# Optimization experiments

Hardware: AMD Instinct MI355X
Metric: run time of the kernel (lower is better)

Reference implementation:

```python
import jax, jax.numpy as jnp
import numpy as np

N_HEAD = 16
T_THRESHOLD = 0.001


def setup_inputs() -> dict:
    key = jax.random.key(0)
    k_x, k_wa, k_ba, k_wp, k_bp = jax.random.split(key, 5)
    B, P, L, R = 8, 1024, 4, 256
    C = L * R  # n_embd = 1024
    s = 1.0 / np.sqrt(C)
    return {
        "x": jax.random.normal(k_x, (B, P, L, R), dtype=jnp.float32),
        "w_attn": jax.random.normal(k_wa, (C, 3 * C), dtype=jnp.float32) * s,
        "b_attn": jax.random.normal(k_ba, (3 * C,), dtype=jnp.float32) * 0.01,
        "w_proj": jax.random.normal(k_wp, (C, C), dtype=jnp.float32) * s,
        "b_proj": jax.random.normal(k_bp, (C,), dtype=jnp.float32) * 0.01,
    }


def reference(x, w_attn, b_attn, w_proj, b_proj):
    B, P, L, R = x.shape
    C = L * R
    H = N_HEAD
    hd = C // H
    xf = x.reshape(B, P, C)                      # (B, T, C)
    qkv = xf @ w_attn + b_attn                   # (B, T, 3C)
    q, k, v = jnp.split(qkv, 3, axis=-1)
    # (B, H, T, hd)
    q = q.reshape(B, P, H, hd).transpose(0, 2, 1, 3)
    k = k.reshape(B, P, H, hd).transpose(0, 2, 1, 3)
    v = v.reshape(B, P, H, hd).transpose(0, 2, 1, 3)
    att = jnp.einsum("bhqd,bhkd->bhqk", q, k) * (1.0 / np.sqrt(hd))
    att = jax.nn.softmax(att, axis=-1)
    att = jax.nn.relu(att - T_THRESHOLD)         # post-softmax thresholding
    y = jnp.einsum("bhqk,bhkd->bhqd", att, v)    # (B, H, T, hd)
    y = y.transpose(0, 2, 1, 3).reshape(B, P, C)
    y = y @ w_proj + b_proj
    return y.reshape(B, P, L, R)
```

## Files before the change

### kernel.cpp

```cpp
#include <hip/hip_runtime.h>


typedef _Float16 half8 __attribute__((ext_vector_type(8)));
typedef _Float16 half4_t __attribute__((ext_vector_type(4)));
typedef float floatx4 __attribute__((ext_vector_type(4)));

__device__ __forceinline__ void gl2lds16(const void* gsrc, void* lds) {
    __builtin_amdgcn_global_load_lds(
        (const __attribute__((address_space(1))) unsigned int*)gsrc,
        (__attribute__((address_space(3))) unsigned int*)lds,
        16, 0, 0);
}

__global__ __launch_bounds__(256) void conv_x(const float4* __restrict__ in,
                                              _Float16* __restrict__ out, int n4) {
    int idx = blockIdx.x * blockDim.x + threadIdx.x;
    int stride = gridDim.x * blockDim.x;
    for (int i = idx; i < n4; i += stride) {
        float4 v = in[i];
        half4_t h = { (_Float16)v.x, (_Float16)v.y, (_Float16)v.z, (_Float16)v.w };
        *(half4_t*)(out + (size_t)i * 4) = h;
    }
}

__global__ __launch_bounds__(256) void tconv(const float* __restrict__ in,
                                             _Float16* __restrict__ out, int R, int C) {
    __shared__ _Float16 t[64 * 65];
    int bx = blockIdx.x, by = blockIdx.y;
#pragma unroll
    for (int it = 0; it < 16; ++it) {
        int idx = it * 256 + threadIdx.x;
        int r = idx >> 6, c = idx & 63;
        t[c * 65 + r] = (_Float16)in[(size_t)(by * 64 + r) * C + bx * 64 + c];
    }
    __syncthreads();
#pragma unroll
    for (int it = 0; it < 16; ++it) {
        int idx = it * 256 + threadIdx.x;
        int rn = idx >> 6, ck = idx & 63;
        out[(size_t)(bx * 64 + rn) * R + by * 64 + ck] = t[rn * 65 + ck];
    }
}


#define GBAR __builtin_amdgcn_s_barrier()
#define WLGKM do { asm volatile("s_waitcnt lgkmcnt(0)" ::: "memory"); } while (0)
#define WVM2  do { asm volatile("s_waitcnt vmcnt(2)"   ::: "memory"); } while (0)
#define WVM0  do { asm volatile("s_waitcnt vmcnt(0)"   ::: "memory"); } while (0)

#define LDA(buf, rg)                                                                          \
    do {                                                                                      \
        _Pragma("unroll") for (int i = 0; i < 2; ++i) {                                       \
            int r_ = wm * 64 + ((rg) * 2 + i) * 16 + l15;                                     \
            _Pragma("unroll") for (int kk = 0; kk < 2; ++kk)                                  \
                a[i][kk] = *(const half8*)(sA + (buf) * 32768 + r_ * 128 +                    \
                                           ((((kk << 2) + quad) ^ (r_ & 7)) << 4));           \
        }                                                                                     \
    } while (0)

#define LDB(buf, cg, bb)                                                                      \
    do {                                                                                      \
        _Pragma("unroll") for (int j = 0; j < 2; ++j) {                                       \
            int r_ = wn * 64 + ((cg) * 2 + j) * 16 + l15;                                     \
            _Pragma("unroll") for (int kk = 0; kk < 2; ++kk)                                  \
                bb[j][kk] = *(const half8*)(sB + (buf) * 16384 + r_ * 128 +                   \
                                            ((((kk << 2) + quad) ^ (r_ & 7)) << 4));          \
        }                                                                                     \
    } while (0)

#define MMA(rg, cg, bb)                                                                       \
    do {                                                                                      \
        __builtin_amdgcn_s_setprio(1);                                                        \
        _Pragma("unroll") for (int kk = 0; kk < 2; ++kk)                                      \
            _Pragma("unroll") for (int i = 0; i < 2; ++i)                                     \
                _Pragma("unroll") for (int j = 0; j < 2; ++j)                                  \
                    acc[(rg) * 2 + i][(cg) * 2 + j] = __builtin_amdgcn_mfma_f32_16x16x32_f16( \
                        a[i][kk], bb[j][kk], acc[(rg) * 2 + i][(cg) * 2 + j], 0, 0, 0);       \
        __builtin_amdgcn_s_setprio(0);                                                        \
    } while (0)

template <bool SPLIT3>
__global__ __launch_bounds__(512, 2) void gemm8p(const _Float16* __restrict__ A,
                                                 const _Float16* __restrict__ BT,
                                                 const float* __restrict__ bias,
                                                 void* __restrict__ o0, void* __restrict__ o1,
                                                 void* __restrict__ o2, int N) {
    __shared__ __attribute__((aligned(16))) char lds[98304];
    char* sA = lds;
    char* sB = lds + 65536;
    int tid = threadIdx.x;
    int W = tid >> 6, lane = tid & 63, quad = lane >> 4, l15 = lane & 15;
    int wm = W >> 1, wn = W & 1;
    int m0 = blockIdx.y * 256, n0 = blockIdx.x * 128;

    auto stA = [&](int buf, int half, int k0) {
#pragma unroll
        for (int rnd = 0; rnd < 2; ++rnd) {
            int c = rnd * 512 + tid;
            int row = c >> 3;
            int q = (c & 7) ^ (row & 7);
            const _Float16* src = A + (size_t)(m0 + half * 128 + row) * 1024 + k0 + q * 8;
            int off = __builtin_amdgcn_readfirstlane(buf * 32768 + half * 16384 +
                                                     rnd * 8192 + (W << 10));
            gl2lds16(src, sA + off);
        }
    };
    auto stB = [&](int buf, int half, int k0) {
        int row = tid >> 3;
        int q = (tid & 7) ^ (row & 7);
        const _Float16* src = BT + (size_t)(n0 + half * 64 + row) * 1024 + k0 + q * 8;
        int off = __builtin_amdgcn_readfirstlane(buf * 16384 + half * 8192 + (W << 10));
        gl2lds16(src, sB + off);
    };

    half8 a[2][2], b0[2][2], b1[2][2];
    floatx4 acc[4][4] = {};

    stA(0, 0, 0); stA(0, 1, 0);
    stB(0, 0, 0); stB(0, 1, 0);
    stB(1, 0, 64); stB(1, 1, 64);
    WVM2;
    GBAR;

#pragma unroll 1
    for (int t = 0; t < 16; t += 2) {
        int k1 = (t + 1) << 6;
        int k2 = ((t + 2) & 15) << 6;
        int k3 = ((t + 3) & 15) << 6;
        LDA(0, 0); LDB(0, 0, b0); stA(1, 0, k1);
        GBAR; WLGKM; MMA(0, 0, b0); GBAR;
        LDB(0, 1, b1); stA(1, 1, k1);
        GBAR; WLGKM; MMA(0, 1, b1); GBAR;
        LDA(0, 1); stB(0, 0, k2);
        GBAR; WLGKM; MMA(1, 1, b1); GBAR;
        stB(0, 1, k2); WVM2;
        GBAR; WLGKM; MMA(1, 0, b0); GBAR;
        LDA(1, 0); LDB(1, 0, b0); stA(0, 0, k2);
        GBAR; WLGKM; MMA(0, 0, b0); GBAR;
        LDB(1, 1, b1); stA(0, 1, k2);
        GBAR; WLGKM; MMA(0, 1, b1); GBAR;
        LDA(1, 1); stB(1, 0, k3);
        GBAR; WLGKM; MMA(1, 1, b1); GBAR;
        stB(1, 1, k3); WVM2;
        GBAR; WLGKM; MMA(1, 0, b0); GBAR;
    }

    if constexpr (!SPLIT3) {
#pragma unroll
        for (int cf = 0; cf < 4; ++cf) {
            int gn = n0 + wn * 64 + cf * 16 + l15;
            float bv = bias[gn];
#pragma unroll
            for (int rf = 0; rf < 4; ++rf) {
                int gmBase = m0 + wm * 64 + rf * 16 + quad * 4;
#pragma unroll
                for (int r = 0; r < 4; ++r)
                    ((float*)o0)[(size_t)(gmBase + r) * N + gn] = acc[rf][cf][r] + bv;
            }
        }
    } else {
        WVM0;
        GBAR;
        int sec = n0 >> 10;
        int nb = n0 & 1023;
        int b = m0 >> 10;
        int tb = m0 & 1023;
        _Float16* qno = (_Float16*)o0;
        _Float16* kPo = (_Float16*)o1;
        _Float16* vPo = (_Float16*)o2;
        if (sec == 2) {
#pragma unroll
            for (int cf = 0; cf < 4; ++cf) {
                int n = wn * 64 + cf * 16 + l15;
                float bv = bias[n0 + n];
#pragma unroll
                for (int rf = 0; rf < 4; ++rf) {
                    int m = wm * 64 + rf * 16 + quad * 4;
                    half4_t h4;
#pragma unroll
                    for (int r = 0; r < 4; ++r) h4[r] = (_Float16)(acc[rf][cf][r] + bv);
                    *(half4_t*)(lds + n * 528 + ((m >> 3) << 4) + (m & 7) * 2) = h4;
                }
            }
            __syncthreads();
            int l15v = tid & 15;
            int moct = W * 4 + ((tid >> 4) & 3);
            int t = tb + moct * 8;
            int kbv = (t >> 5) & 31, quad_v = (t >> 3) & 3;
#pragma unroll
            for (int i = 0; i < 8; ++i) {
                int hh = i >> 2, cf = i & 3;
                int n = hh * 64 + cf * 16 + l15v;
                half8 v = *(const half8*)(lds + n * 528 + (moct << 4));
                int gcol = nb + n;
                int h = gcol >> 6, d = gcol & 63;
                size_t chunk = (size_t)((b * 16 + h) * 32 + kbv) * 256 +
                               (d >> 4) * 64 + quad_v * 16 + (d & 15);
                *(half8*)(vPo + chunk * 8) = v;
            }
        } else {
#pragma unroll
            for (int cf = 0; cf < 4; ++cf) {
                int n = wn * 64 + cf * 16 + l15;
                float bv = bias[n0 + n];
                int nbyte = ((n >> 3) << 4) + (n & 7) * 2;
#pragma unroll
                for (int rf = 0; rf < 4; ++rf) {
                    int m = wm * 64 + rf * 16 + quad * 4;
#pragma unroll
                    for (int r = 0; r < 4; ++r)
                        *(_Float16*)(lds + (m + r) * 272 + nbyte) =
                            (_Float16)(acc[rf][cf][r] + bv);
                }
            }
            __syncthreads();
            if (sec == 0) {
                int noct = tid & 15;
#pragma unroll
                for (int i = 0; i < 8; ++i) {
                    int m = i * 32 + (tid >> 4);
                    half8 v = *(const half8*)(lds + m * 272 + (noct << 4));
                    *(half8*)(qno + (size_t)(b * 1024 + tb + m) * 1024 + nb + noct * 8) = v;
                }
            } else {
                int l15k = tid & 15, noct = (tid >> 4) & 15;
#pragma unroll
                for (int i = 0; i < 8; ++i) {
                    int mb = i * 2 + (tid >> 8);
                    int m = mb * 16 + l15k;
                    half8 v = *(const half8*)(lds + m * 272 + (noct << 4));
                    int gcol = nb + noct * 8;
                    int h = gcol >> 6, d0 = gcol & 63;
                    int t = tb + m;
                    size_t chunk = (size_t)((b * 16 + h) * 64 + (t >> 4)) * 128 +
                                   (d0 >> 5) * 64 + ((d0 >> 3) & 3) * 16 + l15k;
                    *(half8*)(kPo + chunk * 8) = v;
                }
            }
        }
    }
}

__device__ __forceinline__ int esw(int row, int colByte) {
    return row * 2048 + (colByte ^ ((row & 7) << 4));
}

__global__ __launch_bounds__(512, 4) void attn(const _Float16* __restrict__ qn,
                                               const _Float16* __restrict__ kP,
                                               const _Float16* __restrict__ vP,
                                               _Float16* __restrict__ y) {
    __shared__ __attribute__((aligned(16))) _Float16 E[32 * 1024];
    __shared__ float lsum[8][32];
    char* Eb = (char*)E;
    int tid = threadIdx.x;
    int W = tid >> 6, lane = tid & 63, quad = lane >> 4, l15 = lane & 15;
    int flat = blockIdx.y * 32 + blockIdx.x;
    int swz = (flat & 7) * 512 + (flat >> 3);
    int qt = swz & 31, bh = swz >> 5;
    int b = bh >> 4, h = bh & 15;
    int q0 = qt * 32;

    half8 bq[2][2];
#pragma unroll
    for (int nf = 0; nf < 2; ++nf)
#pragma unroll
        for (int ks = 0; ks < 2; ++ks)
            bq[nf][ks] = *(const half8*)(qn + (size_t)(b * 1024 + q0 + nf * 16 + l15) * 1024 +
                                         h * 64 + ks * 32 + quad * 8);

    float lpart[2] = {0.f, 0.f};
#pragma unroll 4
    for (int mt = 0; mt < 8; ++mt) {
        int kb = W * 8 + mt;
        const _Float16* kp = kP + ((size_t)(bh * 64 + kb) * 128 + lane) * 8;
        half8 ak0 = *(const half8*)(kp);
        half8 ak1 = *(const half8*)(kp + 512);
#pragma unroll
        for (int nf = 0; nf < 2; ++nf) {
            floatx4 s = {};
            s = __builtin_amdgcn_mfma_f32_16x16x32_f16(ak0, bq[nf][0], s, 0, 0, 0);
            s = __builtin_amdgcn_mfma_f32_16x16x32_f16(ak1, bq[nf][1], s, 0, 0, 0);
            half4_t h4;
#pragma unroll
            for (int r = 0; r < 4; ++r) {
                float e = __expf(fminf(s[r] * 0.125f, 10.0f));
                lpart[nf] += e;
                h4[r] = (_Float16)e;
            }
            int q = nf * 16 + l15;
            int kbyte = (W * 128 + mt * 16 + quad * 4) * 2;
            *(half4_t*)(Eb + q * 2048 + (kbyte ^ ((q & 7) << 4))) = h4;
        }
    }
#pragma unroll
    for (int nf = 0; nf < 2; ++nf) {
        lpart[nf] += __shfl_xor(lpart[nf], 16);
        lpart[nf] += __shfl_xor(lpart[nf], 32);
    }
    if (lane < 16) {
        lsum[W][l15] = lpart[0];
        lsum[W][16 + l15] = lpart[1];
    }
    __syncthreads();

    half8 inv8[2], t8, z8;
#pragma unroll
    for (int j = 0; j < 8; ++j) { t8[j] = (_Float16)(-0.001f); z8[j] = (_Float16)0.f; }
#pragma unroll
    for (int rf = 0; rf < 2; ++rf) {
        float l = 0.f;
#pragma unroll
        for (int w = 0; w < 8; ++w) l += lsum[w][rf * 16 + l15];
        _Float16 invh = (_Float16)(1.0f / l);
#pragma unroll
        for (int j = 0; j < 8; ++j) inv8[rf][j] = invh;
    }

    floatx4 acc[2][4] = {};
#pragma unroll
    for (int kt = 0; kt < 4; ++kt) {
        int kk = W * 128 + kt * 32;
        half8 ap[2];
#pragma unroll
        for (int rf = 0; rf < 2; ++rf) {
            ap[rf] = *(const half8*)(Eb + esw(rf * 16 + l15, (kk + quad * 8) * 2));
            ap[rf] = ap[rf] * inv8[rf] + t8;
            ap[rf] = __builtin_elementwise_max(ap[rf], z8);
        }
        const _Float16* vbase = vP + ((size_t)(bh * 32 + (W * 4 + kt)) * 256 + lane) * 8;
        half8 bv[4];
#pragma unroll
        for (int cf = 0; cf < 4; ++cf)
            bv[cf] = *(const half8*)(vbase + cf * 512);
#pragma unroll
        for (int rf = 0; rf < 2; ++rf)
#pragma unroll
            for (int cf = 0; cf < 4; ++cf)
                acc[rf][cf] = __builtin_amdgcn_mfma_f32_16x16x32_f16(ap[rf], bv[cf], acc[rf][cf], 0, 0, 0);
    }
    __syncthreads();

    float* red = (float*)E;
#pragma unroll
    for (int rf = 0; rf < 2; ++rf)
#pragma unroll
        for (int cf = 0; cf < 4; ++cf)
#pragma unroll
            for (int r = 0; r < 4; ++r)
                red[W * 2048 + (rf * 16 + quad * 4 + r) * 64 + cf * 16 + l15] = acc[rf][cf][r];
    __syncthreads();
    {
        int e4 = tid * 4;
        int r = e4 >> 6, c = e4 & 63;
        floatx4 s = {};
#pragma unroll
        for (int w = 0; w < 8; ++w) s += *(const floatx4*)(red + w * 2048 + e4);
        half4_t hv = { (_Float16)s[0], (_Float16)s[1], (_Float16)s[2], (_Float16)s[3] };
        *(half4_t*)(y + (size_t)(b * 1024 + q0 + r) * 1024 + h * 64 + c) = hv;
    }
}

extern "C" void kernel_launch(void* const* d_in, const int* in_sizes, int n_in,
                              void* d_out, int out_size, void* d_ws, size_t ws_size,
                              hipStream_t stream) {
    const float* x  = (const float*)d_in[0];
    const float* wa = (const float*)d_in[1];
    const float* ba = (const float*)d_in[2];
    const float* wp = (const float*)d_in[3];
    const float* bp = (const float*)d_in[4];
    float* out = (float*)d_out;

    char* ws = (char*)d_ws;
    _Float16* y   = (_Float16*)(ws);
    _Float16* qn  = (_Float16*)(ws + 16777216);
    _Float16* kP  = (_Float16*)(ws + 33554432);
    _Float16* vP  = (_Float16*)(ws + 50331648);
    _Float16* waT = (_Float16*)(ws + 67108864);
    _Float16* wpT = (_Float16*)(ws + 73400320);
    _Float16* xh  = (_Float16*)(ws + 75497472);

    conv_x<<<4096, 256, 0, stream>>>((const float4*)x, xh, 8388608 / 4);
    tconv<<<dim3(48, 16), 256, 0, stream>>>(wa, waT, 1024, 3072);
    tconv<<<dim3(16, 16), 256, 0, stream>>>(wp, wpT, 1024, 1024);
    gemm8p<true><<<dim3(24, 32), 512, 0, stream>>>(xh, waT, ba, (void*)qn, (void*)kP, (void*)vP, 3072);
    attn<<<dim3(32, 128), 512, 0, stream>>>(qn, kP, vP, y);
    gemm8p<false><<<dim3(8, 32), 512, 0, stream>>>(y, wpT, bp, (void*)out, nullptr, nullptr, 1024);
}
```

Baseline: 260.2 us.

## Use 256x256 tiles for QKV GEMM, merge weight transposes, use exp2 in softmax

The QKV projection moves to a dedicated kernel with 256x256 output tiles, 128 KB of LDS and a 2x4 warp layout. Its epilogue is staged through LDS in two passes so the tile fits. This raises operand reuse per block but halves the grid to 384 blocks and uses more registers per thread, which may hurt occupancy. The two weight-transpose launches are merged into one kernel, and the attention exponent switches from __expf to exp2 with prescaled constants.

```diff
diff --git a/kernel.cpp b/kernel.cpp
--- a/kernel.cpp
+++ b/kernel.cpp
@@ -23,10 +23,14 @@
     }
 }
 
-__global__ __launch_bounds__(256) void tconv(const float* __restrict__ in,
-                                             _Float16* __restrict__ out, int R, int C) {
+__global__ __launch_bounds__(256) void tconv2(const float* __restrict__ wa,
+                                              _Float16* __restrict__ waT,
+                                              const float* __restrict__ wp,
+                                              _Float16* __restrict__ wpT) {
     __shared__ _Float16 t[64 * 65];
     int bx = blockIdx.x, by = blockIdx.y;
+    const float* in = wa; _Float16* out = waT; int C = 3072;
+    if (bx >= 48) { bx -= 48; in = wp; out = wpT; C = 1024; }
 #pragma unroll
     for (int it = 0; it < 16; ++it) {
         int idx = it * 256 + threadIdx.x;
@@ -38,15 +42,204 @@
     for (int it = 0; it < 16; ++it) {
         int idx = it * 256 + threadIdx.x;
         int rn = idx >> 6, ck = idx & 63;
-        out[(size_t)(bx * 64 + rn) * R + by * 64 + ck] = t[rn * 65 + ck];
-    }
-}
-
+        out[(size_t)(bx * 64 + rn) * 1024 + by * 64 + ck] = t[rn * 65 + ck];
+    }
+}
 
 #define GBAR __builtin_amdgcn_s_barrier()
 #define WLGKM do { asm volatile("s_waitcnt lgkmcnt(0)" ::: "memory"); } while (0)
 #define WVM2  do { asm volatile("s_waitcnt vmcnt(2)"   ::: "memory"); } while (0)
+#define WVM4  do { asm volatile("s_waitcnt vmcnt(4)"   ::: "memory"); } while (0)
 #define WVM0  do { asm volatile("s_waitcnt vmcnt(0)"   ::: "memory"); } while (0)
+
+
+#define WLDA(buf, rg)                                                                         \
+    do {                                                                                      \
+        _Pragma("unroll") for (int i = 0; i < 4; ++i) {                                       \
+            int r_ = wm * 128 + ((rg) * 4 + i) * 16 + l15;                                    \
+            _Pragma("unroll") for (int kk = 0; kk < 2; ++kk)                                  \
+                a[i][kk] = *(const half8*)(sA + (buf) * 32768 + r_ * 128 +                    \
+                                           ((((kk << 2) + quad) ^ (r_ & 7)) << 4));           \
+        }                                                                                     \
+    } while (0)
+
+#define WLDB(buf, cg, bb)                                                                     \
+    do {                                                                                      \
+        _Pragma("unroll") for (int j = 0; j < 2; ++j) {                                       \
+            int r_ = wn * 64 + ((cg) * 2 + j) * 16 + l15;                                     \
+            _Pragma("unroll") for (int kk = 0; kk < 2; ++kk)                                  \
+                bb[j][kk] = *(const half8*)(sB + (buf) * 32768 + r_ * 128 +                   \
+                                            ((((kk << 2) + quad) ^ (r_ & 7)) << 4));          \
+        }                                                                                     \
+    } while (0)
+
+#define WMMA(rg, cg, bb)                                                                      \
+    do {                                                                                      \
+        __builtin_amdgcn_s_setprio(1);                                                        \
+        _Pragma("unroll") for (int kk = 0; kk < 2; ++kk)                                      \
+            _Pragma("unroll") for (int i = 0; i < 4; ++i)                                     \
+                _Pragma("unroll") for (int j = 0; j < 2; ++j)                                  \
+                    acc[(rg) * 4 + i][(cg) * 2 + j] = __builtin_amdgcn_mfma_f32_16x16x32_f16( \
+                        a[i][kk], bb[j][kk], acc[(rg) * 4 + i][(cg) * 2 + j], 0, 0, 0);       \
+        __builtin_amdgcn_s_setprio(0);                                                        \
+    } while (0)
+
+__global__ __launch_bounds__(512, 2) void gemm_qkv(const _Float16* __restrict__ A,
+                                                   const _Float16* __restrict__ BT,
+                                                   const float* __restrict__ bias,
+                                                   _Float16* __restrict__ qno,
+                                                   _Float16* __restrict__ kPo,
+                                                   _Float16* __restrict__ vPo) {
+    __shared__ __attribute__((aligned(16))) char lds[131072];
+    char* sA = lds;
+    char* sB = lds + 65536;
+    int tid = threadIdx.x;
+    int W = tid >> 6, lane = tid & 63, quad = lane >> 4, l15 = lane & 15;
+    int wm = W >> 2, wn = W & 3;
+    int m0 = blockIdx.y * 256, n0 = blockIdx.x * 256;
+
+    auto stA = [&](int buf, int half, int k0) {
+#pragma unroll
+        for (int rnd = 0; rnd < 2; ++rnd) {
+            int c = rnd * 512 + tid;
+            int row = c >> 3;
+            int q = (c & 7) ^ (row & 7);
+            const _Float16* src = A + (size_t)(m0 + half * 128 + row) * 1024 + k0 + q * 8;
+            int off = __builtin_amdgcn_readfirstlane(buf * 32768 + half * 16384 +
+                                                     rnd * 8192 + (W << 10));
+            gl2lds16(src, sA + off);
+        }
+    };
+    auto stB = [&](int buf, int half, int k0) {
+#pragma unroll
+        for (int rnd = 0; rnd < 2; ++rnd) {
+            int c = rnd * 512 + tid;
+            int row = c >> 3;
+            int q = (c & 7) ^ (row & 7);
+            const _Float16* src = BT + (size_t)(n0 + half * 128 + row) * 1024 + k0 + q * 8;
+            int off = __builtin_amdgcn_readfirstlane(buf * 32768 + half * 16384 +
+                                                     rnd * 8192 + (W << 10));
+            gl2lds16(src, sB + off);
+        }
+    };
+
+    half8 a[4][2], b0[2][2], b1[2][2];
+    floatx4 acc[8][4] = {};
+
+    stA(0, 0, 0); stA(0, 1, 0);
+    stB(0, 0, 0); stB(0, 1, 0);
+    stB(1, 0, 64); stB(1, 1, 64);
+    WVM4;
+    GBAR;
+
+#pragma unroll 1
+    for (int t = 0; t < 16; t += 2) {
+        int k1 = (t + 1) << 6;
+        int k2 = ((t + 2) & 15) << 6;
+        int k3 = ((t + 3) & 15) << 6;
+        WLDA(0, 0); WLDB(0, 0, b0); stA(1, 0, k1);
+        GBAR; WLGKM; WMMA(0, 0, b0); GBAR;
+        WLDB(0, 1, b1); stA(1, 1, k1);
+        GBAR; WLGKM; WMMA(0, 1, b1); GBAR;
+        WLDA(0, 1); stB(0, 0, k2);
+        GBAR; WLGKM; WMMA(1, 1, b1); GBAR;
+        stB(0, 1, k2); WVM4;
+        GBAR; WLGKM; WMMA(1, 0, b0); GBAR;
+        WLDA(1, 0); WLDB(1, 0, b0); stA(0, 0, k2);
+        GBAR; WLGKM; WMMA(0, 0, b0); GBAR;
+        WLDB(1, 1, b1); stA(0, 1, k2);
+        GBAR; WLGKM; WMMA(0, 1, b1); GBAR;
+        WLDA(1, 1); stB(1, 0, k3);
+        GBAR; WLGKM; WMMA(1, 1, b1); GBAR;
+        stB(1, 1, k3); WVM4;
+        GBAR; WLGKM; WMMA(1, 0, b0); GBAR;
+    }
+
+    WVM0;
+    GBAR;
+    int sec = n0 >> 10;
+    int b = m0 >> 10;
+    int tb = m0 & 1023;
+#pragma unroll 1
+    for (int p = 0; p < 2; ++p) {
+        if (p) __syncthreads();
+        if (sec == 2) {
+            if ((wn >> 1) == p) {
+#pragma unroll
+                for (int cf = 0; cf < 4; ++cf) {
+                    int lc = (wn & 1) * 64 + cf * 16 + l15;
+                    float bv = bias[n0 + wn * 64 + cf * 16 + l15];
+#pragma unroll
+                    for (int rf = 0; rf < 8; ++rf) {
+                        int m = wm * 128 + rf * 16 + quad * 4;
+                        half4_t h4;
+#pragma unroll
+                        for (int r = 0; r < 4; ++r) h4[r] = (_Float16)(acc[rf][cf][r] + bv);
+                        *(half4_t*)(lds + lc * 528 + m * 2) = h4;
+                    }
+                }
+            }
+            __syncthreads();
+            int l15v = tid & 15;
+            int moct = W * 4 + ((tid >> 4) & 3);
+            int t = tb + moct * 8;
+            int kbv = (t >> 5) & 31, quad_v = (t >> 3) & 3;
+            int nbV = (n0 & 1023) + p * 128;
+#pragma unroll
+            for (int i = 0; i < 8; ++i) {
+                int hh = i >> 2, cf = i & 3;
+                int n = hh * 64 + cf * 16 + l15v;
+                half8 v = *(const half8*)(lds + n * 528 + (moct << 4));
+                int gcol = nbV + n;
+                int h = gcol >> 6, d = gcol & 63;
+                size_t chunk = (size_t)((b * 16 + h) * 32 + kbv) * 256 +
+                               (d >> 4) * 64 + quad_v * 16 + (d & 15);
+                *(half8*)(vPo + chunk * 8) = v;
+            }
+        } else {
+            if ((wn >> 1) == p) {
+#pragma unroll
+                for (int cf = 0; cf < 4; ++cf) {
+                    int lc = (wn & 1) * 64 + cf * 16 + l15;
+                    float bv = bias[n0 + wn * 64 + cf * 16 + l15];
+#pragma unroll
+                    for (int rf = 0; rf < 8; ++rf) {
+                        int m = wm * 128 + rf * 16 + quad * 4;
+#pragma unroll
+                        for (int r = 0; r < 4; ++r)
+                            *(_Float16*)(lds + (m + r) * 272 + lc * 2) =
+                                (_Float16)(acc[rf][cf][r] + bv);
+                    }
+                }
+            }
+            __syncthreads();
+            int nb = (n0 & 1023) + p * 128;
+            if (sec == 0) {
+                int noct = tid & 15;
+#pragma unroll
+                for (int i = 0; i < 8; ++i) {
+                    int m = i * 32 + (tid >> 4);
+                    half8 v = *(const half8*)(lds + m * 272 + (noct << 4));
+                    *(half8*)(qno + (size_t)(b * 1024 + tb + m) * 1024 + nb + noct * 8) = v;
+                }
+            } else {
+                int l15k = tid & 15, noct = (tid >> 4) & 15;
+#pragma unroll
+                for (int i = 0; i < 8; ++i) {
+                    int mb = i * 2 + (tid >> 8);
+                    int m = mb * 16 + l15k;
+                    half8 v = *(const half8*)(lds + m * 272 + (noct << 4));
+                    int gcol = nb + noct * 8;
+                    int h = gcol >> 6, d0 = gcol & 63;
+                    int t = tb + m;
+                    size_t chunk = (size_t)((b * 16 + h) * 64 + (t >> 4)) * 128 +
+                                   (d0 >> 5) * 64 + ((d0 >> 3) & 3) * 16 + l15k;
+                    *(half8*)(kPo + chunk * 8) = v;
+                }
+            }
+        }
+    }
+}
 
 #define LDA(buf, rg)                                                                          \
     do {                                                                                      \
@@ -79,12 +272,10 @@
         __builtin_amdgcn_s_setprio(0);                                                        \
     } while (0)
 
-template <bool SPLIT3>
-__global__ __launch_bounds__(512, 2) void gemm8p(const _Float16* __restrict__ A,
-                                                 const _Float16* __restrict__ BT,
-                                                 const float* __restrict__ bias,
-                                                 void* __restrict__ o0, void* __restrict__ o1,
-                                                 void* __restrict__ o2, int N) {
+__global__ __launch_bounds__(512, 2) void gemm_proj(const _Float16* __restrict__ A,
+                                                    const _Float16* __restrict__ BT,
+                                                    const float* __restrict__ bias,
+                                                    float* __restrict__ o0, int N) {
     __shared__ __attribute__((aligned(16))) char lds[98304];
     char* sA = lds;
     char* sB = lds + 65536;
@@ -145,98 +336,16 @@
         GBAR; WLGKM; MMA(1, 0, b0); GBAR;
     }
 
-    if constexpr (!SPLIT3) {
-#pragma unroll
-        for (int cf = 0; cf < 4; ++cf) {
-            int gn = n0 + wn * 64 + cf * 16 + l15;
-            float bv = bias[gn];
-#pragma unroll
-            for (int rf = 0; rf < 4; ++rf) {
-                int gmBase = m0 + wm * 64 + rf * 16 + quad * 4;
-#pragma unroll
-                for (int r = 0; r < 4; ++r)
-                    ((float*)o0)[(size_t)(gmBase + r) * N + gn] = acc[rf][cf][r] + bv;
-            }
-        }
-    } else {
-        WVM0;
-        GBAR;
-        int sec = n0 >> 10;
-        int nb = n0 & 1023;
-        int b = m0 >> 10;
-        int tb = m0 & 1023;
-        _Float16* qno = (_Float16*)o0;
-        _Float16* kPo = (_Float16*)o1;
-        _Float16* vPo = (_Float16*)o2;
-        if (sec == 2) {
-#pragma unroll
-            for (int cf = 0; cf < 4; ++cf) {
-                int n = wn * 64 + cf * 16 + l15;
-                float bv = bias[n0 + n];
-#pragma unroll
-                for (int rf = 0; rf < 4; ++rf) {
-                    int m = wm * 64 + rf * 16 + quad * 4;
-                    half4_t h4;
-#pragma unroll
-                    for (int r = 0; r < 4; ++r) h4[r] = (_Float16)(acc[rf][cf][r] + bv);
-                    *(half4_t*)(lds + n * 528 + ((m >> 3) << 4) + (m & 7) * 2) = h4;
-                }
-            }
-            __syncthreads();
-            int l15v = tid & 15;
-            int moct = W * 4 + ((tid >> 4) & 3);
-            int t = tb + moct * 8;
-            int kbv = (t >> 5) & 31, quad_v = (t >> 3) & 3;
-#pragma unroll
-            for (int i = 0; i < 8; ++i) {
-                int hh = i >> 2, cf = i & 3;
-                int n = hh * 64 + cf * 16 + l15v;
-                half8 v = *(const half8*)(lds + n * 528 + (moct << 4));
-                int gcol = nb + n;
-                int h = gcol >> 6, d = gcol & 63;
-                size_t chunk = (size_t)((b * 16 + h) * 32 + kbv) * 256 +
-                               (d >> 4) * 64 + quad_v * 16 + (d & 15);
-                *(half8*)(vPo + chunk * 8) = v;
-            }
-        } else {
-#pragma unroll
-            for (int cf = 0; cf < 4; ++cf) {
-                int n = wn * 64 + cf * 16 + l15;
-                float bv = bias[n0 + n];
-                int nbyte = ((n >> 3) << 4) + (n & 7) * 2;
-#pragma unroll
-                for (int rf = 0; rf < 4; ++rf) {
-                    int m = wm * 64 + rf * 16 + quad * 4;
-#pragma unroll
-                    for (int r = 0; r < 4; ++r)
-                        *(_Float16*)(lds + (m + r) * 272 + nbyte) =
-                            (_Float16)(acc[rf][cf][r] + bv);
-                }
-            }
-            __syncthreads();
-            if (sec == 0) {
-                int noct = tid & 15;
-#pragma unroll
-                for (int i = 0; i < 8; ++i) {
-                    int m = i * 32 + (tid >> 4);
-                    half8 v = *(const half8*)(lds + m * 272 + (noct << 4));
-                    *(half8*)(qno + (size_t)(b * 1024 + tb + m) * 1024 + nb + noct * 8) = v;
-                }
-            } else {
-                int l15k = tid & 15, noct = (tid >> 4) & 15;
-#pragma unroll
-                for (int i = 0; i < 8; ++i) {
-                    int mb = i * 2 + (tid >> 8);
-                    int m = mb * 16 + l15k;
-                    half8 v = *(const half8*)(lds + m * 272 + (noct << 4));
-                    int gcol = nb + noct * 8;
-                    int h = gcol >> 6, d0 = gcol & 63;
-                    int t = tb + m;
-                    size_t chunk = (size_t)((b * 16 + h) * 64 + (t >> 4)) * 128 +
-                                   (d0 >> 5) * 64 + ((d0 >> 3) & 3) * 16 + l15k;
-                    *(half8*)(kPo + chunk * 8) = v;
-                }
-            }
+#pragma unroll
+    for (int cf = 0; cf < 4; ++cf) {
+        int gn = n0 + wn * 64 + cf * 16 + l15;
+        float bv = bias[gn];
+#pragma unroll
+        for (int rf = 0; rf < 4; ++rf) {
+            int gmBase = m0 + wm * 64 + rf * 16 + quad * 4;
+#pragma unroll
+            for (int r = 0; r < 4; ++r)
+                o0[(size_t)(gmBase + r) * N + gn] = acc[rf][cf][r] + bv;
         }
     }
 }
@@ -283,7 +392,7 @@
             half4_t h4;
 #pragma unroll
             for (int r = 0; r < 4; ++r) {
-                float e = __expf(fminf(s[r] * 0.125f, 10.0f));
+                float e = __builtin_amdgcn_exp2f(fminf(s[r] * 0.18033688f, 14.4269504f));
                 lpart[nf] += e;
                 h4[r] = (_Float16)e;
             }
@@ -380,9 +489,8 @@
     _Float16* xh  = (_Float16*)(ws + 75497472);
 
     conv_x<<<4096, 256, 0, stream>>>((const float4*)x, xh, 8388608 / 4);
-    tconv<<<dim3(48, 16), 256, 0, stream>>>(wa, waT, 1024, 3072);
-    tconv<<<dim3(16, 16), 256, 0, stream>>>(wp, wpT, 1024, 1024);
-    gemm8p<true><<<dim3(24, 32), 512, 0, stream>>>(xh, waT, ba, (void*)qn, (void*)kP, (void*)vP, 3072);
+    tconv2<<<dim3(64, 16), 256, 0, stream>>>(wa, waT, wp, wpT);
+    gemm_qkv<<<dim3(12, 32), 512, 0, stream>>>(xh, waT, ba, qn, kP, vP);
     attn<<<dim3(32, 128), 512, 0, stream>>>(qn, kP, vP, y);
-    gemm8p<false><<<dim3(8, 32), 512, 0, stream>>>(y, wpT, bp, (void*)out, nullptr, nullptr, 1024);
-}
+    gemm_proj<<<dim3(8, 32), 512, 0, stream>>>(y, wpT, bp, out, 1024);
+}
```

Result: no change. 258.3 us (-0.7%).
